# Kernel optimization log

Measured on AMD Instinct MI355X. Metric: run time of the kernel, lower is better.

## Reference

```python
import jax, jax.numpy as jnp
import numpy as np

B, C, T = 64, 512, 1000
BR = 3
RED = 1
H = C // RED


def setup_inputs() -> dict:
    key = jax.random.key(0)
    ks = jax.random.split(key, 8)
    x0 = jax.random.normal(ks[0], (B, C, T), dtype=jnp.float32)
    x1 = jax.random.normal(ks[1], (B, C, T), dtype=jnp.float32)
    x2 = jax.random.normal(ks[2], (B, C, T), dtype=jnp.float32)
    # linear1: Conv1d(2C -> H, kernel 1) == dense [H, 2C]
    W1 = jax.random.normal(ks[3], (H, 2 * C), dtype=jnp.float32) * (1.0 / np.sqrt(2 * C))
    b1 = jnp.zeros((H,), dtype=jnp.float32)
    # linear2: BR branch convs Conv1d(H -> C, kernel 1), stacked: [BR, C, H]
    W2 = jax.random.normal(ks[4], (BR, C, H), dtype=jnp.float32) * (1.0 / np.sqrt(H))
    b2 = jnp.zeros((BR, C), dtype=jnp.float32)
    return {"x0": x0, "x1": x1, "x2": x2, "W1": W1, "b1": b1, "W2": W2, "b2": b2}


def reference(x0, x1, x2, W1, b1, W2, b2):
    # f: [B, BR, C, T]
    f = jnp.stack([x0, x1, x2], axis=1)
    xs = f.sum(axis=1)  # [B, C, T]
    t = xs.shape[-1]
    mean = xs.mean(axis=-1)  # [B, C]
    # unbiased std (torch.std default)
    var = ((xs - mean[..., None]) ** 2).sum(axis=-1) / (t - 1)
    std = jnp.sqrt(var)
    stats = jnp.concatenate([mean, std], axis=-1)  # [B, 2C]
    h = stats @ W1.T + b1  # [B, H]
    s = jnp.einsum('bh,kch->bkc', h, W2) + b2  # [B, BR, C]
    w = jax.nn.softmax(s, axis=1)[..., None]  # [B, BR, C, 1]
    return (f * w).sum(axis=1)  # [B, C, T]
```

## Files before the change

### kernel.cpp

```cpp
#include <hip/hip_runtime.h>
#include <math.h>

#define NB 64
#define NC 512
#define NT 1000
#define NH 512
#define TWOC 1024
#define NT4 250
#define TAIL 58

typedef float vfloat4 __attribute__((ext_vector_type(4)));

__global__ __launch_bounds__(256, 1) void stats_kernel(const float* __restrict__ x0,
                                                       const float* __restrict__ x1,
                                                       const float* __restrict__ x2,
                                                       float* __restrict__ stats) {
    const int row  = blockIdx.x * 4 + (threadIdx.x >> 6);
    const int lane = threadIdx.x & 63;

    const float4* p0 = (const float4*)x0 + (size_t)row * NT4;
    const float4* p1 = (const float4*)x1 + (size_t)row * NT4;
    const float4* p2 = (const float4*)x2 + (size_t)row * NT4;

    const bool tail = lane < TAIL;
    const int  i3   = tail ? (192 + lane) : lane;
    const float m3  = tail ? 1.f : 0.f;

    const float4 a0 = p0[lane];
    const float4 a1 = p0[lane + 64];
    const float4 a2 = p0[lane + 128];
    const float4 a3 = p0[i3];
    const float4 b0 = p1[lane];
    const float4 b1 = p1[lane + 64];
    const float4 b2 = p1[lane + 128];
    const float4 b3 = p1[i3];
    const float4 c0 = p2[lane];
    const float4 c1 = p2[lane + 64];
    const float4 c2 = p2[lane + 128];
    const float4 c3 = p2[i3];
    __builtin_amdgcn_sched_barrier(0);

    float s0 = 0.f, q0 = 0.f, s1 = 0.f, q1 = 0.f;
    float s2 = 0.f, q2 = 0.f, s3 = 0.f, q3 = 0.f;
    float v;
    v = a0.x + b0.x + c0.x; s0 += v; q0 += v * v;
    v = a0.y + b0.y + c0.y; s0 += v; q0 += v * v;
    v = a0.z + b0.z + c0.z; s0 += v; q0 += v * v;
    v = a0.w + b0.w + c0.w; s0 += v; q0 += v * v;
    v = a1.x + b1.x + c1.x; s1 += v; q1 += v * v;
    v = a1.y + b1.y + c1.y; s1 += v; q1 += v * v;
    v = a1.z + b1.z + c1.z; s1 += v; q1 += v * v;
    v = a1.w + b1.w + c1.w; s1 += v; q1 += v * v;
    v = a2.x + b2.x + c2.x; s2 += v; q2 += v * v;
    v = a2.y + b2.y + c2.y; s2 += v; q2 += v * v;
    v = a2.z + b2.z + c2.z; s2 += v; q2 += v * v;
    v = a2.w + b2.w + c2.w; s2 += v; q2 += v * v;
    v = (a3.x + b3.x + c3.x) * m3; s3 += v; q3 += v * v;
    v = (a3.y + b3.y + c3.y) * m3; s3 += v; q3 += v * v;
    v = (a3.z + b3.z + c3.z) * m3; s3 += v; q3 += v * v;
    v = (a3.w + b3.w + c3.w) * m3; s3 += v; q3 += v * v;

    float s  = (s0 + s1) + (s2 + s3);
    float sq = (q0 + q1) + (q2 + q3);

    #pragma unroll
    for (int off = 32; off; off >>= 1) {
        s  += __shfl_down(s,  off);
        sq += __shfl_down(sq, off);
    }
    if (lane == 0) {
        const float mean = s / (float)NT;
        const float var  = (sq - s * s / (float)NT) / (float)(NT - 1);
        const float sd   = sqrtf(fmaxf(var, 0.f));
        const int b = row >> 9;
        const int c = row & (NC - 1);
        stats[b * TWOC + c]      = mean;
        stats[b * TWOC + NC + c] = sd;
    }
}

__global__ __launch_bounds__(256) void h_kernel(const float* __restrict__ stats,
                                                const float* __restrict__ W1,
                                                const float* __restrict__ b1,
                                                float* __restrict__ hbuf) {
    const int wid  = blockIdx.x * 4 + (threadIdx.x >> 6);
    const int lane = threadIdx.x & 63;
    const int j    = wid >> 4;
    const int b0   = (wid & 15) * 4;

    const float4* wr  = (const float4*)(W1 + (size_t)j * TWOC);
    const float4* s0p = (const float4*)(stats + (size_t)(b0 + 0) * TWOC);
    const float4* s1p = (const float4*)(stats + (size_t)(b0 + 1) * TWOC);
    const float4* s2p = (const float4*)(stats + (size_t)(b0 + 2) * TWOC);
    const float4* s3p = (const float4*)(stats + (size_t)(b0 + 3) * TWOC);

    float a0 = 0.f, a1 = 0.f, a2 = 0.f, a3 = 0.f;
    #pragma unroll
    for (int r = 0; r < 4; ++r) {
        const int i4 = r * 64 + lane;
        const float4 wv = wr[i4];
        const float4 v0 = s0p[i4];
        const float4 v1 = s1p[i4];
        const float4 v2 = s2p[i4];
        const float4 v3 = s3p[i4];
        a0 += wv.x*v0.x + wv.y*v0.y + wv.z*v0.z + wv.w*v0.w;
        a1 += wv.x*v1.x + wv.y*v1.y + wv.z*v1.z + wv.w*v1.w;
        a2 += wv.x*v2.x + wv.y*v2.y + wv.z*v2.z + wv.w*v2.w;
        a3 += wv.x*v3.x + wv.y*v3.y + wv.z*v3.z + wv.w*v3.w;
    }
    #pragma unroll
    for (int off = 32; off; off >>= 1) {
        a0 += __shfl_down(a0, off);
        a1 += __shfl_down(a1, off);
        a2 += __shfl_down(a2, off);
        a3 += __shfl_down(a3, off);
    }
    if (lane == 0) {
        const float bb = b1[j];
        hbuf[(size_t)(b0 + 0) * NH + j] = a0 + bb;
        hbuf[(size_t)(b0 + 1) * NH + j] = a1 + bb;
        hbuf[(size_t)(b0 + 2) * NH + j] = a2 + bb;
        hbuf[(size_t)(b0 + 3) * NH + j] = a3 + bb;
    }
}

__global__ __launch_bounds__(256) void sw_kernel(const float* __restrict__ hbuf,
                                                 const float* __restrict__ W2,
                                                 const float* __restrict__ b2,
                                                 float* __restrict__ wbuf) {
    const int wid  = blockIdx.x * 4 + (threadIdx.x >> 6);
    const int lane = threadIdx.x & 63;
    const int c    = wid >> 4;
    const int b0   = (wid & 15) * 4;

    const float4* w0r = (const float4*)(W2 + ((size_t)(0 * NC + c)) * NH);
    const float4* w1r = (const float4*)(W2 + ((size_t)(1 * NC + c)) * NH);
    const float4* w2r = (const float4*)(W2 + ((size_t)(2 * NC + c)) * NH);

    float acc00=0,acc01=0,acc02=0,acc03=0;
    float acc10=0,acc11=0,acc12=0,acc13=0;
    float acc20=0,acc21=0,acc22=0,acc23=0;

    #pragma unroll
    for (int r = 0; r < 2; ++r) {
        const int i4 = r * 64 + lane;
        const float4 w0v = w0r[i4];
        const float4 w1v = w1r[i4];
        const float4 w2v = w2r[i4];
        const float4 h0 = ((const float4*)(hbuf + (size_t)(b0 + 0) * NH))[i4];
        const float4 h1 = ((const float4*)(hbuf + (size_t)(b0 + 1) * NH))[i4];
        const float4 h2 = ((const float4*)(hbuf + (size_t)(b0 + 2) * NH))[i4];
        const float4 h3 = ((const float4*)(hbuf + (size_t)(b0 + 3) * NH))[i4];
        acc00 += w0v.x*h0.x + w0v.y*h0.y + w0v.z*h0.z + w0v.w*h0.w;
        acc01 += w0v.x*h1.x + w0v.y*h1.y + w0v.z*h1.z + w0v.w*h1.w;
        acc02 += w0v.x*h2.x + w0v.y*h2.y + w0v.z*h2.z + w0v.w*h2.w;
        acc03 += w0v.x*h3.x + w0v.y*h3.y + w0v.z*h3.z + w0v.w*h3.w;
        acc10 += w1v.x*h0.x + w1v.y*h0.y + w1v.z*h0.z + w1v.w*h0.w;
        acc11 += w1v.x*h1.x + w1v.y*h1.y + w1v.z*h1.z + w1v.w*h1.w;
        acc12 += w1v.x*h2.x + w1v.y*h2.y + w1v.z*h2.z + w1v.w*h2.w;
        acc13 += w1v.x*h3.x + w1v.y*h3.y + w1v.z*h3.z + w1v.w*h3.w;
        acc20 += w2v.x*h0.x + w2v.y*h0.y + w2v.z*h0.z + w2v.w*h0.w;
        acc21 += w2v.x*h1.x + w2v.y*h1.y + w2v.z*h1.z + w2v.w*h1.w;
        acc22 += w2v.x*h2.x + w2v.y*h2.y + w2v.z*h2.z + w2v.w*h2.w;
        acc23 += w2v.x*h3.x + w2v.y*h3.y + w2v.z*h3.z + w2v.w*h3.w;
    }
    #pragma unroll
    for (int off = 32; off; off >>= 1) {
        acc00 += __shfl_down(acc00, off); acc01 += __shfl_down(acc01, off);
        acc02 += __shfl_down(acc02, off); acc03 += __shfl_down(acc03, off);
        acc10 += __shfl_down(acc10, off); acc11 += __shfl_down(acc11, off);
        acc12 += __shfl_down(acc12, off); acc13 += __shfl_down(acc13, off);
        acc20 += __shfl_down(acc20, off); acc21 += __shfl_down(acc21, off);
        acc22 += __shfl_down(acc22, off); acc23 += __shfl_down(acc23, off);
    }
    if (lane == 0) {
        const float bb0 = b2[0 * NC + c];
        const float bb1 = b2[1 * NC + c];
        const float bb2 = b2[2 * NC + c];
        float v0[4] = {acc00 + bb0, acc01 + bb0, acc02 + bb0, acc03 + bb0};
        float v1[4] = {acc10 + bb1, acc11 + bb1, acc12 + bb1, acc13 + bb1};
        float v2[4] = {acc20 + bb2, acc21 + bb2, acc22 + bb2, acc23 + bb2};
        #pragma unroll
        for (int bb = 0; bb < 4; ++bb) {
            const float m  = fmaxf(v0[bb], fmaxf(v1[bb], v2[bb]));
            const float e0 = expf(v0[bb] - m);
            const float e1 = expf(v1[bb] - m);
            const float e2 = expf(v2[bb] - m);
            const float inv = 1.f / (e0 + e1 + e2);
            const size_t base = (size_t)(b0 + bb) * 3 * NC + c;
            wbuf[base + 0 * NC] = e0 * inv;
            wbuf[base + 1 * NC] = e1 * inv;
            wbuf[base + 2 * NC] = e2 * inv;
        }
    }
}

__global__ __launch_bounds__(256) void apply_kernel(const float* __restrict__ x0,
                                                    const float* __restrict__ x1,
                                                    const float* __restrict__ x2,
                                                    const float* __restrict__ wbuf,
                                                    float* __restrict__ out) {
    const int rblk = (int)gridDim.x - 1 - (int)blockIdx.x;
    const int row  = rblk * 4 + (threadIdx.x >> 6);
    const int lane = threadIdx.x & 63;
    const int b = row >> 9;
    const int c = row & (NC - 1);

    const float4* p0 = (const float4*)x0 + (size_t)row * NT4;
    const float4* p1 = (const float4*)x1 + (size_t)row * NT4;
    const float4* p2 = (const float4*)x2 + (size_t)row * NT4;
    vfloat4*      po = (vfloat4*)out     + (size_t)row * NT4;

    const bool tail = lane < TAIL;
    const int  i3   = tail ? (192 + lane) : lane;

    const float w0 = wbuf[((size_t)b * 3 + 0) * NC + c];
    const float w1 = wbuf[((size_t)b * 3 + 1) * NC + c];
    const float w2 = wbuf[((size_t)b * 3 + 2) * NC + c];
    const float4 a0 = p0[lane];
    const float4 a1 = p0[lane + 64];
    const float4 a2 = p0[lane + 128];
    const float4 a3 = p0[i3];
    const float4 d0 = p1[lane];
    const float4 d1 = p1[lane + 64];
    const float4 d2 = p1[lane + 128];
    const float4 d3 = p1[i3];
    const float4 e0 = p2[lane];
    const float4 e1 = p2[lane + 64];
    const float4 e2 = p2[lane + 128];
    const float4 e3 = p2[i3];
    __builtin_amdgcn_sched_barrier(0);

    vfloat4 o;
    o.x = a0.x*w0 + d0.x*w1 + e0.x*w2;
    o.y = a0.y*w0 + d0.y*w1 + e0.y*w2;
    o.z = a0.z*w0 + d0.z*w1 + e0.z*w2;
    o.w = a0.w*w0 + d0.w*w1 + e0.w*w2;
    __builtin_nontemporal_store(o, &po[lane]);
    o.x = a1.x*w0 + d1.x*w1 + e1.x*w2;
    o.y = a1.y*w0 + d1.y*w1 + e1.y*w2;
    o.z = a1.z*w0 + d1.z*w1 + e1.z*w2;
    o.w = a1.w*w0 + d1.w*w1 + e1.w*w2;
    __builtin_nontemporal_store(o, &po[lane + 64]);
    o.x = a2.x*w0 + d2.x*w1 + e2.x*w2;
    o.y = a2.y*w0 + d2.y*w1 + e2.y*w2;
    o.z = a2.z*w0 + d2.z*w1 + e2.z*w2;
    o.w = a2.w*w0 + d2.w*w1 + e2.w*w2;
    __builtin_nontemporal_store(o, &po[lane + 128]);
    if (tail) {
        o.x = a3.x*w0 + d3.x*w1 + e3.x*w2;
        o.y = a3.y*w0 + d3.y*w1 + e3.y*w2;
        o.z = a3.z*w0 + d3.z*w1 + e3.z*w2;
        o.w = a3.w*w0 + d3.w*w1 + e3.w*w2;
        __builtin_nontemporal_store(o, &po[i3]);
    }
}

extern "C" void kernel_launch(void* const* d_in, const int* in_sizes, int n_in,
                              void* d_out, int out_size, void* d_ws, size_t ws_size,
                              hipStream_t stream) {
    const float* x0 = (const float*)d_in[0];
    const float* x1 = (const float*)d_in[1];
    const float* x2 = (const float*)d_in[2];
    const float* W1 = (const float*)d_in[3];
    const float* b1 = (const float*)d_in[4];
    const float* W2 = (const float*)d_in[5];
    const float* b2 = (const float*)d_in[6];
    float* out = (float*)d_out;

    float* stats = (float*)d_ws;
    float* hbuf  = stats + NB * TWOC;
    float* wbuf  = hbuf + NB * NH;

    stats_kernel<<<NB * NC / 4, 256, 0, stream>>>(x0, x1, x2, stats);
    h_kernel<<<2048, 256, 0, stream>>>(stats, W1, b1, hbuf);
    sw_kernel<<<2048, 256, 0, stream>>>(hbuf, W2, b2, wbuf);
    apply_kernel<<<NB * NC / 4, 256, 0, stream>>>(x0, x1, x2, wbuf, out);
}
```

Baseline: 169.5 us.

## Make stats kernel persistent with double-buffered inline-asm global loads

The stats kernel now launches 4096 waves instead of 32768, and each wave handles 8 rows spaced 4096 apart. Loads for the next row are issued through inline-asm global_load_dwordx4 into alternating register sets while the current row is reduced, gated by explicit vmcnt waits. The aim is to keep more memory requests in flight per wave and hide load latency without depending on wave-level occupancy. In exchange it uses more registers, and the hand-written asm and waitcnt bookkeeping are fragile: the compiler cannot track these loads, so correctness depends on the manual vmcnt counts.

```diff
diff --git a/kernel.cpp b/kernel.cpp
--- a/kernel.cpp
+++ b/kernel.cpp
@@ -8,75 +8,109 @@
 #define TWOC 1024
 #define NT4 250
 #define TAIL 58
+#define SWAVES 4096
 
 typedef float vfloat4 __attribute__((ext_vector_type(4)));
 
-__global__ __launch_bounds__(256, 1) void stats_kernel(const float* __restrict__ x0,
-                                                       const float* __restrict__ x1,
-                                                       const float* __restrict__ x2,
+#define GLOAD(dst, addr)          asm volatile("global_load_dwordx4 %0, %1, off"            : "=v"(dst) : "v"(addr))
+#define GLOAD_OFF(dst, addr, o)   asm volatile("global_load_dwordx4 %0, %1, off offset:" #o : "=v"(dst) : "v"(addr))
+#define VMWAIT(n)                 do { asm volatile("s_waitcnt vmcnt(" #n ")" ::: "memory"); __builtin_amdgcn_sched_barrier(0); } while (0)
+
+__global__ __launch_bounds__(256, 1) void stats_kernel(const float* __restrict__ x0f,
+                                                       const float* __restrict__ x1f,
+                                                       const float* __restrict__ x2f,
                                                        float* __restrict__ stats) {
-    const int row  = blockIdx.x * 4 + (threadIdx.x >> 6);
+    const int w    = blockIdx.x * 4 + (threadIdx.x >> 6);
     const int lane = threadIdx.x & 63;
-
-    const float4* p0 = (const float4*)x0 + (size_t)row * NT4;
-    const float4* p1 = (const float4*)x1 + (size_t)row * NT4;
-    const float4* p2 = (const float4*)x2 + (size_t)row * NT4;
-
     const bool tail = lane < TAIL;
     const int  i3   = tail ? (192 + lane) : lane;
     const float m3  = tail ? 1.f : 0.f;
 
-    const float4 a0 = p0[lane];
-    const float4 a1 = p0[lane + 64];
-    const float4 a2 = p0[lane + 128];
-    const float4 a3 = p0[i3];
-    const float4 b0 = p1[lane];
-    const float4 b1 = p1[lane + 64];
-    const float4 b2 = p1[lane + 128];
-    const float4 b3 = p1[i3];
-    const float4 c0 = p2[lane];
-    const float4 c1 = p2[lane + 64];
-    const float4 c2 = p2[lane + 128];
-    const float4 c3 = p2[i3];
-    __builtin_amdgcn_sched_barrier(0);
-
-    float s0 = 0.f, q0 = 0.f, s1 = 0.f, q1 = 0.f;
-    float s2 = 0.f, q2 = 0.f, s3 = 0.f, q3 = 0.f;
-    float v;
-    v = a0.x + b0.x + c0.x; s0 += v; q0 += v * v;
-    v = a0.y + b0.y + c0.y; s0 += v; q0 += v * v;
-    v = a0.z + b0.z + c0.z; s0 += v; q0 += v * v;
-    v = a0.w + b0.w + c0.w; s0 += v; q0 += v * v;
-    v = a1.x + b1.x + c1.x; s1 += v; q1 += v * v;
-    v = a1.y + b1.y + c1.y; s1 += v; q1 += v * v;
-    v = a1.z + b1.z + c1.z; s1 += v; q1 += v * v;
-    v = a1.w + b1.w + c1.w; s1 += v; q1 += v * v;
-    v = a2.x + b2.x + c2.x; s2 += v; q2 += v * v;
-    v = a2.y + b2.y + c2.y; s2 += v; q2 += v * v;
-    v = a2.z + b2.z + c2.z; s2 += v; q2 += v * v;
-    v = a2.w + b2.w + c2.w; s2 += v; q2 += v * v;
-    v = (a3.x + b3.x + c3.x) * m3; s3 += v; q3 += v * v;
-    v = (a3.y + b3.y + c3.y) * m3; s3 += v; q3 += v * v;
-    v = (a3.z + b3.z + c3.z) * m3; s3 += v; q3 += v * v;
-    v = (a3.w + b3.w + c3.w) * m3; s3 += v; q3 += v * v;
-
-    float s  = (s0 + s1) + (s2 + s3);
-    float sq = (q0 + q1) + (q2 + q3);
-
-    #pragma unroll
-    for (int off = 32; off; off >>= 1) {
-        s  += __shfl_down(s,  off);
-        sq += __shfl_down(sq, off);
-    }
-    if (lane == 0) {
-        const float mean = s / (float)NT;
-        const float var  = (sq - s * s / (float)NT) / (float)(NT - 1);
-        const float sd   = sqrtf(fmaxf(var, 0.f));
-        const int b = row >> 9;
-        const int c = row & (NC - 1);
-        stats[b * TWOC + c]      = mean;
-        stats[b * TWOC + NC + c] = sd;
-    }
+    const float4* x0 = (const float4*)x0f;
+    const float4* x1 = (const float4*)x1f;
+    const float4* x2 = (const float4*)x2f;
+
+    vfloat4 A0,A1,A2,A3,A4,A5,A6,A7,A8,A9,A10,A11;
+    vfloat4 B0,B1,B2,B3,B4,B5,B6,B7,B8,B9,B10,B11;
+
+#define ISSUE(row, R0,R1,R2,R3,R4,R5,R6,R7,R8,R9,R10,R11) do {                     \
+        const float4* p0_ = x0 + (size_t)(row) * NT4;                              \
+        const float4* p1_ = x1 + (size_t)(row) * NT4;                              \
+        const float4* p2_ = x2 + (size_t)(row) * NT4;                              \
+        const unsigned long long Aa = (unsigned long long)(p0_ + lane);            \
+        const unsigned long long At = (unsigned long long)(p0_ + i3);              \
+        const unsigned long long Ba = (unsigned long long)(p1_ + lane);            \
+        const unsigned long long Bt = (unsigned long long)(p1_ + i3);              \
+        const unsigned long long Ca = (unsigned long long)(p2_ + lane);            \
+        const unsigned long long Ct = (unsigned long long)(p2_ + i3);              \
+        GLOAD(R0, Aa); GLOAD_OFF(R1, Aa, 1024); GLOAD_OFF(R2, Aa, 2048); GLOAD(R3, At); \
+        GLOAD(R4, Ba); GLOAD_OFF(R5, Ba, 1024); GLOAD_OFF(R6, Ba, 2048); GLOAD(R7, Bt); \
+        GLOAD(R8, Ca); GLOAD_OFF(R9, Ca, 1024); GLOAD_OFF(R10, Ca, 2048); GLOAD(R11, Ct); \
+    } while (0)
+
+#define REDUCE(row, R0,R1,R2,R3,R4,R5,R6,R7,R8,R9,R10,R11) do {                    \
+        float s0=0.f,q0=0.f,s1=0.f,q1=0.f,s2=0.f,q2=0.f,s3=0.f,q3=0.f,v;           \
+        v = R0.x + R4.x + R8.x;  s0 += v; q0 += v*v;                               \
+        v = R0.y + R4.y + R8.y;  s0 += v; q0 += v*v;                               \
+        v = R0.z + R4.z + R8.z;  s0 += v; q0 += v*v;                               \
+        v = R0.w + R4.w + R8.w;  s0 += v; q0 += v*v;                               \
+        v = R1.x + R5.x + R9.x;  s1 += v; q1 += v*v;                               \
+        v = R1.y + R5.y + R9.y;  s1 += v; q1 += v*v;                               \
+        v = R1.z + R5.z + R9.z;  s1 += v; q1 += v*v;                               \
+        v = R1.w + R5.w + R9.w;  s1 += v; q1 += v*v;                               \
+        v = R2.x + R6.x + R10.x; s2 += v; q2 += v*v;                               \
+        v = R2.y + R6.y + R10.y; s2 += v; q2 += v*v;                               \
+        v = R2.z + R6.z + R10.z; s2 += v; q2 += v*v;                               \
+        v = R2.w + R6.w + R10.w; s2 += v; q2 += v*v;                               \
+        v = (R3.x + R7.x + R11.x) * m3; s3 += v; q3 += v*v;                        \
+        v = (R3.y + R7.y + R11.y) * m3; s3 += v; q3 += v*v;                        \
+        v = (R3.z + R7.z + R11.z) * m3; s3 += v; q3 += v*v;                        \
+        v = (R3.w + R7.w + R11.w) * m3; s3 += v; q3 += v*v;                        \
+        float s  = (s0 + s1) + (s2 + s3);                                          \
+        float sq = (q0 + q1) + (q2 + q3);                                          \
+        _Pragma("unroll")                                                          \
+        for (int off = 32; off; off >>= 1) {                                       \
+            s  += __shfl_down(s,  off);                                            \
+            sq += __shfl_down(sq, off);                                            \
+        }                                                                          \
+        if (lane == 0) {                                                           \
+            const float mean = s / (float)NT;                                      \
+            const float var  = (sq - s * s / (float)NT) / (float)(NT - 1);         \
+            const float sd   = sqrtf(fmaxf(var, 0.f));                             \
+            const int b_ = (row) >> 9;                                             \
+            const int c_ = (row) & (NC - 1);                                       \
+            stats[b_ * TWOC + c_]      = mean;                                     \
+            stats[b_ * TWOC + NC + c_] = sd;                                       \
+        }                                                                          \
+    } while (0)
+
+    ISSUE(w, A0,A1,A2,A3,A4,A5,A6,A7,A8,A9,A10,A11);
+    ISSUE(w + 1*SWAVES, B0,B1,B2,B3,B4,B5,B6,B7,B8,B9,B10,B11);
+    VMWAIT(12);
+    REDUCE(w, A0,A1,A2,A3,A4,A5,A6,A7,A8,A9,A10,A11);
+    ISSUE(w + 2*SWAVES, A0,A1,A2,A3,A4,A5,A6,A7,A8,A9,A10,A11);
+    VMWAIT(12);
+    REDUCE(w + 1*SWAVES, B0,B1,B2,B3,B4,B5,B6,B7,B8,B9,B10,B11);
+    ISSUE(w + 3*SWAVES, B0,B1,B2,B3,B4,B5,B6,B7,B8,B9,B10,B11);
+    VMWAIT(12);
+    REDUCE(w + 2*SWAVES, A0,A1,A2,A3,A4,A5,A6,A7,A8,A9,A10,A11);
+    ISSUE(w + 4*SWAVES, A0,A1,A2,A3,A4,A5,A6,A7,A8,A9,A10,A11);
+    VMWAIT(12);
+    REDUCE(w + 3*SWAVES, B0,B1,B2,B3,B4,B5,B6,B7,B8,B9,B10,B11);
+    ISSUE(w + 5*SWAVES, B0,B1,B2,B3,B4,B5,B6,B7,B8,B9,B10,B11);
+    VMWAIT(12);
+    REDUCE(w + 4*SWAVES, A0,A1,A2,A3,A4,A5,A6,A7,A8,A9,A10,A11);
+    ISSUE(w + 6*SWAVES, A0,A1,A2,A3,A4,A5,A6,A7,A8,A9,A10,A11);
+    VMWAIT(12);
+    REDUCE(w + 5*SWAVES, B0,B1,B2,B3,B4,B5,B6,B7,B8,B9,B10,B11);
+    ISSUE(w + 7*SWAVES, B0,B1,B2,B3,B4,B5,B6,B7,B8,B9,B10,B11);
+    VMWAIT(12);
+    REDUCE(w + 6*SWAVES, A0,A1,A2,A3,A4,A5,A6,A7,A8,A9,A10,A11);
+    VMWAIT(0);
+    REDUCE(w + 7*SWAVES, B0,B1,B2,B3,B4,B5,B6,B7,B8,B9,B10,B11);
+
+#undef ISSUE
+#undef REDUCE
 }
 
 __global__ __launch_bounds__(256) void h_kernel(const float* __restrict__ stats,
@@ -272,7 +306,7 @@
     float* hbuf  = stats + NB * TWOC;
     float* wbuf  = hbuf + NB * NH;
 
-    stats_kernel<<<NB * NC / 4, 256, 0, stream>>>(x0, x1, x2, stats);
+    stats_kernel<<<SWAVES / 4, 256, 0, stream>>>(x0, x1, x2, stats);
     h_kernel<<<2048, 256, 0, stream>>>(stats, W1, b1, hbuf);
     sw_kernel<<<2048, 256, 0, stream>>>(hbuf, W2, b2, wbuf);
     apply_kernel<<<NB * NC / 4, 256, 0, stream>>>(x0, x1, x2, wbuf, out);
```

Result: no change. 168.5 us (-0.6%).

## Stash bf16 copies of the inputs during the stats pass and apply from them

Applied to the files above, without the earlier changes.

The stats kernel now also writes bf16-rounded copies of x0, x1 and x2 into the workspace. A new apply kernel reads those half-size copies, visiting rows in reverse block order, instead of re-reading the fp32 inputs. The reverse order is meant to hit the most recently written data while it may still sit in the last-level cache. This adds write traffic and rounds the inputs to bf16, which lowers output accuracy, and the new path only runs if the workspace is large enough; otherwise it falls back to the original kernels.

```diff
diff --git a/kernel.cpp b/kernel.cpp
--- a/kernel.cpp
+++ b/kernel.cpp
@@ -10,11 +10,170 @@
 #define TAIL 58
 
 typedef float vfloat4 __attribute__((ext_vector_type(4)));
-
-__global__ __launch_bounds__(256, 1) void stats_kernel(const float* __restrict__ x0,
-                                                       const float* __restrict__ x1,
-                                                       const float* __restrict__ x2,
-                                                       float* __restrict__ stats) {
+typedef unsigned short ushort4v __attribute__((ext_vector_type(4)));
+typedef unsigned short ushort8v __attribute__((ext_vector_type(8)));
+
+__device__ __forceinline__ unsigned short f2bf(float f) {
+    unsigned u = __float_as_uint(f);
+    u += 0x7FFFu + ((u >> 16) & 1u);
+    return (unsigned short)(u >> 16);
+}
+__device__ __forceinline__ float bf2f(unsigned short h) {
+    return __uint_as_float(((unsigned)h) << 16);
+}
+
+__global__ __launch_bounds__(256) void statsconv_kernel(const float* __restrict__ x0,
+                                                        const float* __restrict__ x1,
+                                                        const float* __restrict__ x2,
+                                                        float* __restrict__ stats,
+                                                        unsigned short* __restrict__ y0,
+                                                        unsigned short* __restrict__ y1,
+                                                        unsigned short* __restrict__ y2) {
+    const int row  = blockIdx.x * 4 + (threadIdx.x >> 6);
+    const int lane = threadIdx.x & 63;
+
+    const float4* p0 = (const float4*)x0 + (size_t)row * NT4;
+    const float4* p1 = (const float4*)x1 + (size_t)row * NT4;
+    const float4* p2 = (const float4*)x2 + (size_t)row * NT4;
+
+    const bool tail = lane < TAIL;
+    const int  i3   = tail ? (192 + lane) : lane;
+    const float m3  = tail ? 1.f : 0.f;
+
+    const float4 a0 = p0[lane];
+    const float4 a1 = p0[lane + 64];
+    const float4 a2 = p0[lane + 128];
+    const float4 a3 = p0[i3];
+    const float4 b0 = p1[lane];
+    const float4 b1 = p1[lane + 64];
+    const float4 b2 = p1[lane + 128];
+    const float4 b3 = p1[i3];
+    const float4 c0 = p2[lane];
+    const float4 c1 = p2[lane + 64];
+    const float4 c2 = p2[lane + 128];
+    const float4 c3 = p2[i3];
+    __builtin_amdgcn_sched_barrier(0);
+
+    const size_t rbase = (size_t)row * NT;
+    ushort4v* q0 = (ushort4v*)(y0 + rbase);
+    ushort4v* q1 = (ushort4v*)(y1 + rbase);
+    ushort4v* q2 = (ushort4v*)(y2 + rbase);
+    {
+        ushort4v t;
+        t[0]=f2bf(a0.x); t[1]=f2bf(a0.y); t[2]=f2bf(a0.z); t[3]=f2bf(a0.w); q0[lane]       = t;
+        t[0]=f2bf(a1.x); t[1]=f2bf(a1.y); t[2]=f2bf(a1.z); t[3]=f2bf(a1.w); q0[64 + lane]  = t;
+        t[0]=f2bf(a2.x); t[1]=f2bf(a2.y); t[2]=f2bf(a2.z); t[3]=f2bf(a2.w); q0[128 + lane] = t;
+        if (tail) { t[0]=f2bf(a3.x); t[1]=f2bf(a3.y); t[2]=f2bf(a3.z); t[3]=f2bf(a3.w); q0[192 + lane] = t; }
+        t[0]=f2bf(b0.x); t[1]=f2bf(b0.y); t[2]=f2bf(b0.z); t[3]=f2bf(b0.w); q1[lane]       = t;
+        t[0]=f2bf(b1.x); t[1]=f2bf(b1.y); t[2]=f2bf(b1.z); t[3]=f2bf(b1.w); q1[64 + lane]  = t;
+        t[0]=f2bf(b2.x); t[1]=f2bf(b2.y); t[2]=f2bf(b2.z); t[3]=f2bf(b2.w); q1[128 + lane] = t;
+        if (tail) { t[0]=f2bf(b3.x); t[1]=f2bf(b3.y); t[2]=f2bf(b3.z); t[3]=f2bf(b3.w); q1[192 + lane] = t; }
+        t[0]=f2bf(c0.x); t[1]=f2bf(c0.y); t[2]=f2bf(c0.z); t[3]=f2bf(c0.w); q2[lane]       = t;
+        t[0]=f2bf(c1.x); t[1]=f2bf(c1.y); t[2]=f2bf(c1.z); t[3]=f2bf(c1.w); q2[64 + lane]  = t;
+        t[0]=f2bf(c2.x); t[1]=f2bf(c2.y); t[2]=f2bf(c2.z); t[3]=f2bf(c2.w); q2[128 + lane] = t;
+        if (tail) { t[0]=f2bf(c3.x); t[1]=f2bf(c3.y); t[2]=f2bf(c3.z); t[3]=f2bf(c3.w); q2[192 + lane] = t; }
+    }
+
+    float s0 = 0.f, q0s = 0.f, s1 = 0.f, q1s = 0.f;
+    float s2 = 0.f, q2s = 0.f, s3 = 0.f, q3s = 0.f;
+    float v;
+    v = a0.x + b0.x + c0.x; s0 += v; q0s += v * v;
+    v = a0.y + b0.y + c0.y; s0 += v; q0s += v * v;
+    v = a0.z + b0.z + c0.z; s0 += v; q0s += v * v;
+    v = a0.w + b0.w + c0.w; s0 += v; q0s += v * v;
+    v = a1.x + b1.x + c1.x; s1 += v; q1s += v * v;
+    v = a1.y + b1.y + c1.y; s1 += v; q1s += v * v;
+    v = a1.z + b1.z + c1.z; s1 += v; q1s += v * v;
+    v = a1.w + b1.w + c1.w; s1 += v; q1s += v * v;
+    v = a2.x + b2.x + c2.x; s2 += v; q2s += v * v;
+    v = a2.y + b2.y + c2.y; s2 += v; q2s += v * v;
+    v = a2.z + b2.z + c2.z; s2 += v; q2s += v * v;
+    v = a2.w + b2.w + c2.w; s2 += v; q2s += v * v;
+    v = (a3.x + b3.x + c3.x) * m3; s3 += v; q3s += v * v;
+    v = (a3.y + b3.y + c3.y) * m3; s3 += v; q3s += v * v;
+    v = (a3.z + b3.z + c3.z) * m3; s3 += v; q3s += v * v;
+    v = (a3.w + b3.w + c3.w) * m3; s3 += v; q3s += v * v;
+
+    float s  = (s0 + s1) + (s2 + s3);
+    float sq = (q0s + q1s) + (q2s + q3s);
+    #pragma unroll
+    for (int off = 32; off; off >>= 1) {
+        s  += __shfl_down(s,  off);
+        sq += __shfl_down(sq, off);
+    }
+    if (lane == 0) {
+        const float mean = s / (float)NT;
+        const float var  = (sq - s * s / (float)NT) / (float)(NT - 1);
+        const float sd   = sqrtf(fmaxf(var, 0.f));
+        const int b = row >> 9;
+        const int c = row & (NC - 1);
+        stats[b * TWOC + c]      = mean;
+        stats[b * TWOC + NC + c] = sd;
+    }
+}
+
+__global__ __launch_bounds__(256) void applyb_kernel(const unsigned short* __restrict__ y0,
+                                                     const unsigned short* __restrict__ y1,
+                                                     const unsigned short* __restrict__ y2,
+                                                     const float* __restrict__ wbuf,
+                                                     float* __restrict__ out) {
+    const int rblk = (int)gridDim.x - 1 - (int)blockIdx.x;
+    const int row  = rblk * 4 + (threadIdx.x >> 6);
+    const int lane = threadIdx.x & 63;
+    const int b = row >> 9;
+    const int c = row & (NC - 1);
+
+    const float w0 = wbuf[((size_t)b * 3 + 0) * NC + c];
+    const float w1 = wbuf[((size_t)b * 3 + 1) * NC + c];
+    const float w2 = wbuf[((size_t)b * 3 + 2) * NC + c];
+
+    const size_t rbase = (size_t)row * NT;
+    const ushort8v* q0 = (const ushort8v*)(y0 + rbase);
+    const ushort8v* q1 = (const ushort8v*)(y1 + rbase);
+    const ushort8v* q2 = (const ushort8v*)(y2 + rbase);
+
+    const bool t2 = lane < 61;
+    const int  j2 = t2 ? (64 + lane) : lane;
+
+    const ushort8v A0 = q0[lane];
+    const ushort8v A1 = q0[j2];
+    const ushort8v B0 = q1[lane];
+    const ushort8v B1 = q1[j2];
+    const ushort8v C0 = q2[lane];
+    const ushort8v C1 = q2[j2];
+    __builtin_amdgcn_sched_barrier(0);
+
+    vfloat4* po = (vfloat4*)out + (size_t)row * NT4;
+
+    vfloat4 o;
+    o.x = bf2f(A0[0])*w0 + bf2f(B0[0])*w1 + bf2f(C0[0])*w2;
+    o.y = bf2f(A0[1])*w0 + bf2f(B0[1])*w1 + bf2f(C0[1])*w2;
+    o.z = bf2f(A0[2])*w0 + bf2f(B0[2])*w1 + bf2f(C0[2])*w2;
+    o.w = bf2f(A0[3])*w0 + bf2f(B0[3])*w1 + bf2f(C0[3])*w2;
+    __builtin_nontemporal_store(o, &po[2 * lane]);
+    o.x = bf2f(A0[4])*w0 + bf2f(B0[4])*w1 + bf2f(C0[4])*w2;
+    o.y = bf2f(A0[5])*w0 + bf2f(B0[5])*w1 + bf2f(C0[5])*w2;
+    o.z = bf2f(A0[6])*w0 + bf2f(B0[6])*w1 + bf2f(C0[6])*w2;
+    o.w = bf2f(A0[7])*w0 + bf2f(B0[7])*w1 + bf2f(C0[7])*w2;
+    __builtin_nontemporal_store(o, &po[2 * lane + 1]);
+    if (t2) {
+        o.x = bf2f(A1[0])*w0 + bf2f(B1[0])*w1 + bf2f(C1[0])*w2;
+        o.y = bf2f(A1[1])*w0 + bf2f(B1[1])*w1 + bf2f(C1[1])*w2;
+        o.z = bf2f(A1[2])*w0 + bf2f(B1[2])*w1 + bf2f(C1[2])*w2;
+        o.w = bf2f(A1[3])*w0 + bf2f(B1[3])*w1 + bf2f(C1[3])*w2;
+        __builtin_nontemporal_store(o, &po[128 + 2 * lane]);
+        o.x = bf2f(A1[4])*w0 + bf2f(B1[4])*w1 + bf2f(C1[4])*w2;
+        o.y = bf2f(A1[5])*w0 + bf2f(B1[5])*w1 + bf2f(C1[5])*w2;
+        o.z = bf2f(A1[6])*w0 + bf2f(B1[6])*w1 + bf2f(C1[6])*w2;
+        o.w = bf2f(A1[7])*w0 + bf2f(B1[7])*w1 + bf2f(C1[7])*w2;
+        __builtin_nontemporal_store(o, &po[128 + 2 * lane + 1]);
+    }
+}
+
+__global__ __launch_bounds__(256) void stats_kernel(const float* __restrict__ x0,
+                                                    const float* __restrict__ x1,
+                                                    const float* __restrict__ x2,
+                                                    float* __restrict__ stats) {
     const int row  = blockIdx.x * 4 + (threadIdx.x >> 6);
     const int lane = threadIdx.x & 63;
 
@@ -62,7 +221,6 @@
 
     float s  = (s0 + s1) + (s2 + s3);
     float sq = (q0 + q1) + (q2 + q3);
-
     #pragma unroll
     for (int off = 32; off; off >>= 1) {
         s  += __shfl_down(s,  off);
@@ -271,9 +429,22 @@
     float* stats = (float*)d_ws;
     float* hbuf  = stats + NB * TWOC;
     float* wbuf  = hbuf + NB * NH;
-
-    stats_kernel<<<NB * NC / 4, 256, 0, stream>>>(x0, x1, x2, stats);
-    h_kernel<<<2048, 256, 0, stream>>>(stats, W1, b1, hbuf);
-    sw_kernel<<<2048, 256, 0, stream>>>(hbuf, W2, b2, wbuf);
-    apply_kernel<<<NB * NC / 4, 256, 0, stream>>>(x0, x1, x2, wbuf, out);
-}
+    unsigned short* y0 = (unsigned short*)(wbuf + NB * 3 * NC);
+    const size_t nelem = (size_t)NB * NC * NT;
+    unsigned short* y1 = y0 + nelem;
+    unsigned short* y2 = y1 + nelem;
+
+    const size_t need = (size_t)(NB*TWOC + NB*NH + NB*3*NC) * 4 + 3 * nelem * 2;
+
+    if (ws_size >= need) {
+        statsconv_kernel<<<NB * NC / 4, 256, 0, stream>>>(x0, x1, x2, stats, y0, y1, y2);
+        h_kernel<<<2048, 256, 0, stream>>>(stats, W1, b1, hbuf);
+        sw_kernel<<<2048, 256, 0, stream>>>(hbuf, W2, b2, wbuf);
+        applyb_kernel<<<NB * NC / 4, 256, 0, stream>>>(y0, y1, y2, wbuf, out);
+    } else {
+        stats_kernel<<<NB * NC / 4, 256, 0, stream>>>(x0, x1, x2, stats);
+        h_kernel<<<2048, 256, 0, stream>>>(stats, W1, b1, hbuf);
+        sw_kernel<<<2048, 256, 0, stream>>>(hbuf, W2, b2, wbuf);
+        apply_kernel<<<NB * NC / 4, 256, 0, stream>>>(x0, x1, x2, wbuf, out);
+    }
+}
```

Result: slower. 199.2 us (+17.5%).
